# Kernel optimization log

Measured on AMD Instinct MI355X. Metric: run time of the kernel, lower is better.

The kernel has to match this reference:

```python
import jax, jax.numpy as jnp
import numpy as np

HIDDEN = 2048
NUM_HEADS = 16
NUM_KV_HEADS = 4
HEAD_DIM = HIDDEN // NUM_HEADS  # 128
WINDOW = 512
THETA = 10000.0
BATCH = 4
SEQ = 2048
NEG = -1e30


def _apply_rope(x, pos, theta):
    # x: [T, H, D] with interleaved even/odd rotation, matching the torch strided slicing
    half = x.shape[-1] // 2
    inv_freq = 1.0 / (theta ** (jnp.arange(half, dtype=jnp.float32) / half))
    ang = pos.astype(jnp.float32)[:, None] * inv_freq[None, :]          # [T, half]
    cos = jnp.cos(ang)[:, None, :]                                       # [T, 1, half]
    sin = jnp.sin(ang)[:, None, :]
    xe = x[..., 0::2].astype(jnp.float32)
    xo = x[..., 1::2].astype(jnp.float32)
    re = xe * cos - xo * sin
    ro = xe * sin + xo * cos
    out = jnp.stack([re, ro], axis=-1).reshape(x.shape)                  # re-interleave
    return out.astype(x.dtype)


def setup_inputs() -> dict:
    key = jax.random.key(0)
    ks = jax.random.split(key, 5)
    sc = 1.0 / np.sqrt(HIDDEN)
    hidden_states = jax.random.normal(ks[0], (BATCH * SEQ, HIDDEN), dtype=jnp.float32)
    q_w = jax.random.normal(ks[1], (HIDDEN, NUM_HEADS * HEAD_DIM), dtype=jnp.float32) * sc
    k_w = jax.random.normal(ks[2], (HIDDEN, NUM_KV_HEADS * HEAD_DIM), dtype=jnp.float32) * sc
    v_w = jax.random.normal(ks[3], (HIDDEN, NUM_KV_HEADS * HEAD_DIM), dtype=jnp.float32) * sc
    o_w = jax.random.normal(ks[4], (HIDDEN, HIDDEN), dtype=jnp.float32) * sc
    position_ids = jnp.tile(jnp.arange(SEQ, dtype=jnp.int32), BATCH)     # restart per sequence
    cu_seqlens = jnp.arange(BATCH + 1, dtype=jnp.int32) * SEQ
    return {
        "hidden_states": hidden_states, "q_w": q_w, "k_w": k_w, "v_w": v_w, "o_w": o_w,
        "position_ids": position_ids, "cu_seqlens": cu_seqlens, "max_seq_len": SEQ,
    }


def reference(hidden_states, q_w, k_w, v_w, o_w, position_ids, cu_seqlens, max_seq_len):
    T = hidden_states.shape[0]
    B = cu_seqlens.shape[0] - 1
    S = T // B  # equal-length packing
    groups = NUM_HEADS // NUM_KV_HEADS

    q = (hidden_states @ q_w).reshape(T, NUM_HEADS, HEAD_DIM)
    k = (hidden_states @ k_w).reshape(T, NUM_KV_HEADS, HEAD_DIM)
    v = (hidden_states @ v_w).reshape(T, NUM_KV_HEADS, HEAD_DIM)

    q = _apply_rope(q, position_ids, THETA)
    k = _apply_rope(k, position_ids, THETA)

    q = q.reshape(B, S, NUM_HEADS, HEAD_DIM)
    k = k.reshape(B, S, NUM_KV_HEADS, HEAD_DIM)
    v = v.reshape(B, S, NUM_KV_HEADS, HEAD_DIM)
    # GQA: expand kv heads to query heads
    k = jnp.repeat(k, groups, axis=2)   # [B, S, H, D]
    v = jnp.repeat(v, groups, axis=2)

    scale = 1.0 / np.sqrt(HEAD_DIM)
    scores = jnp.einsum('bqhd,bkhd->bhqk', q, k) * scale  # [B, H, S, S]

    pos = position_ids.reshape(B, S)
    pq = pos[:, None, :, None]
    pk = pos[:, None, None, :]
    # causal + sliding window (flash window_size=(WINDOW, 0) semantics): q-k in [0, WINDOW]
    allowed = (pk <= pq) & ((pq - pk) <= WINDOW)
    scores = jnp.where(allowed, scores, NEG)

    probs = jax.nn.softmax(scores, axis=-1)
    attn = jnp.einsum('bhqk,bkhd->bqhd', probs, v)        # [B, S, H, D]
    attn = attn.reshape(T, HIDDEN)
    return attn @ o_w
```

## Files before the change

### kernel.cpp

```cpp
#include <hip/hip_runtime.h>
#include <hip/hip_bf16.h>
#include <cstdint>
#include <cstddef>

typedef __bf16 bf16;
typedef __bf16 bf16x2 __attribute__((ext_vector_type(2)));
typedef __bf16 bf16x8 __attribute__((ext_vector_type(8)));
typedef float  f32x4  __attribute__((ext_vector_type(4)));

#define HIDDEN 2048
#define NHEADS 16
#define NKV    4
#define HD     128
#define WINDOW 512

__device__ __forceinline__ void gld16(const void* g, void* s) {
  __builtin_amdgcn_global_load_lds((const __attribute__((address_space(1))) void*)g,
                                   (__attribute__((address_space(3))) void*)s, 16, 0, 0);
}

__device__ __forceinline__ f32x4 mfma16(bf16x8 a, bf16x8 b, f32x4 c) {
  return __builtin_amdgcn_mfma_f32_16x16x32_bf16(a, b, c, 0, 0, 0);
}

__device__ __forceinline__ void barrier_raw() {
  asm volatile("" ::: "memory");
  __builtin_amdgcn_s_barrier();
  asm volatile("" ::: "memory");
}

__global__ __launch_bounds__(256) void cast_f32_bf16(const float* __restrict__ in,
                                                     bf16* __restrict__ out, int n4) {
  int i = blockIdx.x * 256 + threadIdx.x;
  if (i >= n4) return;
  f32x4 v = *(const f32x4*)(in + (size_t)i * 4);
  bf16x2 a, b;
  a[0] = (bf16)v[0]; a[1] = (bf16)v[1];
  b[0] = (bf16)v[2]; b[1] = (bf16)v[3];
  *(bf16x2*)(out + (size_t)i * 4)     = a;
  *(bf16x2*)(out + (size_t)i * 4 + 2) = b;
}

__global__ __launch_bounds__(256) void transpose_cast(const float* __restrict__ in,
                                                      bf16* __restrict__ out, int R, int C) {
  __shared__ float tile[32][33];
  int c0 = blockIdx.x * 32, r0 = blockIdx.y * 32;
  int tx = threadIdx.x, ty = threadIdx.y;
  #pragma unroll
  for (int i = 0; i < 4; ++i)
    tile[ty + i * 8][tx] = in[(size_t)(r0 + ty + i * 8) * C + c0 + tx];
  __syncthreads();
  #pragma unroll
  for (int i = 0; i < 4; ++i)
    out[(size_t)(c0 + ty + i * 8) * R + r0 + tx] = (bf16)tile[tx][ty + i * 8];
}

__device__ __forceinline__ void stage128x32(const bf16* __restrict__ A,
                                            const bf16* __restrict__ Bt,
                                            bf16* sA, bf16* sB,
                                            int m0, int n0, int K, int kt, int tid) {
  int wbase = tid & ~63;
  #pragma unroll
  for (int r = 0; r < 2; ++r) {
    int e = (r * 256 + tid) * 8;
    int row = e >> 5, col = e & 31;
    gld16(A  + (size_t)(m0 + row) * K + (size_t)kt * 32 + col,
          sA + (size_t)(r * 256 + wbase) * 8);
    gld16(Bt + (size_t)(n0 + row) * K + (size_t)kt * 32 + col,
          sB + (size_t)(r * 256 + wbase) * 8);
  }
}

__global__ __launch_bounds__(256) void gemm_bt(const bf16* __restrict__ A,
                                               const bf16* __restrict__ Bt,
                                               void* __restrict__ Cv,
                                               bf16* __restrict__ Vtout,
                                               int M, int N, int K, int outMode) {
  __shared__ bf16 sA[2][128 * 32];
  __shared__ bf16 sB[2][128 * 32];
  int nb = N >> 7;
  int perx = (int)gridDim.x >> 3;
  int bid0 = (int)blockIdx.x;
  int swzb = (bid0 & 7) * perx + (bid0 >> 3);
  int bm = swzb / nb, bn = swzb % nb;
  int m0 = bm << 7, n0 = bn << 7;
  int tid = threadIdx.x;
  int lane = tid & 63, w = tid >> 6;
  int li = lane & 15, g = lane >> 4, g8 = g * 8;
  int wm = w >> 1, wn = w & 1;
  f32x4 acc[4][4] = {};
  int NT = K >> 5;

  stage128x32(A, Bt, sA[0], sB[0], m0, n0, K, 0, tid);
  for (int kt = 0; kt < NT; ++kt) {
    int cur = kt & 1;
    asm volatile("s_waitcnt vmcnt(0)" ::: "memory");
    barrier_raw();
    if (kt + 1 < NT)
      stage128x32(A, Bt, sA[cur ^ 1], sB[cur ^ 1], m0, n0, K, kt + 1, tid);
    bf16x8 af[4], bv[4];
    #pragma unroll
    for (int mt = 0; mt < 4; ++mt)
      af[mt] = *(const bf16x8*)&sA[cur][(wm * 64 + mt * 16 + li) * 32 + g8];
    #pragma unroll
    for (int nt = 0; nt < 4; ++nt)
      bv[nt] = *(const bf16x8*)&sB[cur][(wn * 64 + nt * 16 + li) * 32 + g8];
    #pragma unroll
    for (int mt = 0; mt < 4; ++mt)
      #pragma unroll
      for (int nt = 0; nt < 4; ++nt)
        acc[mt][nt] = mfma16(af[mt], bv[nt], acc[mt][nt]);
  }
  #pragma unroll
  for (int mt = 0; mt < 4; ++mt)
    #pragma unroll
    for (int nt = 0; nt < 4; ++nt)
      #pragma unroll
      for (int j = 0; j < 4; ++j) {
        int row = m0 + wm * 64 + mt * 16 + g * 4 + j;
        int col = n0 + wn * 64 + nt * 16 + li;
        float v = acc[mt][nt][j];
        if (outMode == 0)      ((bf16*)Cv)[(size_t)row * N + col] = (bf16)v;
        else if (outMode == 1) ((bf16*)Cv)[(size_t)col * M + row] = (bf16)v;
        else if (outMode == 2) ((float*)Cv)[(size_t)row * N + col] = v;
        else {
          if (col < 512) ((bf16*)Cv)[(size_t)row * 512 + col] = (bf16)v;
          else           Vtout[(size_t)(col - 512) * M + row] = (bf16)v;
        }
      }
}

template<int RSP>
__device__ __forceinline__ void stage_quad(const bf16* __restrict__ G,
                                           bf16* __restrict__ sbuf,
                                           int grow0, int K, int k0, int half, int tid) {
  int w = tid >> 6, lane = tid & 63;
  int rl = lane >> 3;
  int col = ((lane & 7) ^ rl) * 8;
  #pragma unroll
  for (int r = 0; r < 2; ++r) {
    int lr0 = r * 64 + w * 8;
    int row0 = (lr0 & (RSP - 1)) + half * RSP + (lr0 / RSP) * 2 * RSP;
    gld16(G + (size_t)(grow0 + row0 + rl) * K + k0 + col,
          sbuf + row0 * 64);
  }
}

__global__ __launch_bounds__(512, 2) void gemm256(const bf16* __restrict__ A,
                                                  const bf16* __restrict__ Bt,
                                                  void* __restrict__ Cv,
                                                  int M, int N, int K, int outMode) {
  __shared__ bf16 sA[2][256 * 64];
  __shared__ bf16 sB[2][256 * 64];
  int nb = N >> 8;
  int cpx = (int)gridDim.x >> 3;
  int bid = (int)blockIdx.x;
  int swzb = (bid & 7) * cpx + (bid >> 3);
  int bm = swzb / nb, bn = swzb % nb;
  int m0 = bm << 8, n0 = bn << 8;
  int tid = threadIdx.x, lane = tid & 63, w = tid >> 6;
  int li = lane & 15, g = lane >> 4;
  int wm = w >> 2, wn = w & 3;
  int swz = (li & 7);

  f32x4 acc[8][4] = {};
  bf16x8 af[4][2];
  bf16x8 bv[2][2][2];

  int NT = K >> 6;

  stage_quad<64>(A,  sA[0], m0, K, 0, 0, tid);
  stage_quad<32>(Bt, sB[0], n0, K, 0, 0, tid);
  stage_quad<32>(Bt, sB[0], n0, K, 0, 1, tid);
  stage_quad<64>(A,  sA[0], m0, K, 0, 1, tid);

#define VMW(n) asm volatile("s_waitcnt vmcnt(" #n ")" ::: "memory")
#define SBAR() __builtin_amdgcn_sched_barrier(0)
#define LGKM(n) { asm volatile("s_waitcnt lgkmcnt(" #n ")" ::: "memory"); \
  __builtin_amdgcn_sched_barrier(0); }
#define LOAD_A256(mh) { _Pragma("unroll") for (int mf = 0; mf < 4; ++mf) \
  _Pragma("unroll") for (int ks = 0; ks < 2; ++ks) { \
    int row = wm * 128 + (mh) * 64 + mf * 16 + li; \
    af[mf][ks] = *(const bf16x8*)&sA[cur][row * 64 + ((ks * 4 + g) ^ swz) * 8]; } }
#define LOAD_B256(nh) { _Pragma("unroll") for (int nf = 0; nf < 2; ++nf) \
  _Pragma("unroll") for (int ks = 0; ks < 2; ++ks) { \
    int row = wn * 64 + (nh) * 32 + nf * 16 + li; \
    bv[nh][nf][ks] = *(const bf16x8*)&sB[cur][row * 64 + ((ks * 4 + g) ^ swz) * 8]; } }
#define MFMA_PH(mh, nh) { \
  __builtin_amdgcn_s_setprio(1); \
  _Pragma("unroll") for (int mf = 0; mf < 4; ++mf) \
  _Pragma("unroll") for (int nf = 0; nf < 2; ++nf) \
  _Pragma("unroll") for (int ks = 0; ks < 2; ++ks) \
    acc[(mh) * 4 + mf][(nh) * 2 + nf] = \
      mfma16(af[mf][ks], bv[nh][nf][ks], acc[(mh) * 4 + mf][(nh) * 2 + nf]); \
  __builtin_amdgcn_s_setprio(0); }

  int cur = 0;
  for (int t = 0; t < NT; ++t) {
    int nxt = cur ^ 1;
    bool pre = (t + 1 < NT);
    int k1 = (t + 1) << 6;
    VMW(0);
    barrier_raw();
    if (pre) stage_quad<64>(A, sA[nxt], m0, K, k1, 0, tid);
    LOAD_A256(0); LOAD_B256(0);
    SBAR();
    LOAD_B256(1);
    if (pre) stage_quad<32>(Bt, sB[nxt], n0, K, k1, 0, tid);
    LGKM(4);
    MFMA_PH(0, 0);
    if (pre) stage_quad<32>(Bt, sB[nxt], n0, K, k1, 1, tid);
    LGKM(0);
    MFMA_PH(0, 1);
    LOAD_A256(1);
    if (pre) stage_quad<64>(A, sA[nxt], m0, K, k1, 1, tid);
    LGKM(0);
    MFMA_PH(1, 1);
    MFMA_PH(1, 0);
    cur = nxt;
  }
#undef VMW
#undef SBAR
#undef LGKM
#undef LOAD_A256
#undef LOAD_B256
#undef MFMA_PH

  #pragma unroll
  for (int mi = 0; mi < 8; ++mi)
    #pragma unroll
    for (int ni = 0; ni < 4; ++ni)
      #pragma unroll
      for (int j = 0; j < 4; ++j) {
        int row = m0 + wm * 128 + mi * 16 + g * 4 + j;
        int col = n0 + wn * 64 + ni * 16 + li;
        float v = acc[mi][ni][j];
        if (outMode == 2) ((float*)Cv)[(size_t)row * N + col] = v;
        else              ((bf16*)Cv)[(size_t)row * N + col] = (bf16)v;
      }
}

__global__ __launch_bounds__(256) void rope_kernel(bf16* __restrict__ X,
                                                   const int* __restrict__ pos,
                                                   int T, int heads) {
  int idx = blockIdx.x * 256 + threadIdx.x;
  int total = T * heads * 64;
  if (idx >= total) return;
  int i = idx & 63;
  int rest = idx >> 6;
  int hh = rest % heads;
  int t = rest / heads;
  float inv = expf((float)i * (-9.210340371976184f / 64.0f));
  float ang = (float)pos[t] * inv;
  float s, c;
  sincosf(ang, &s, &c);
  bf16* p = X + ((size_t)t * heads + hh) * HD + 2 * i;
  bf16x2 xv = *(const bf16x2*)p;
  float xe = (float)xv[0], xo = (float)xv[1];
  bf16x2 r;
  r[0] = (bf16)(xe * c - xo * s);
  r[1] = (bf16)(xe * s + xo * c);
  *(bf16x2*)p = r;
}

__global__ __launch_bounds__(512) void attn_kernel(const bf16* __restrict__ Q,
                                                   const bf16* __restrict__ Kb,
                                                   const bf16* __restrict__ Vt,
                                                   const int* __restrict__ pos,
                                                   const int* __restrict__ cu,
                                                   bf16* __restrict__ O, int T, int B) {
  __shared__ bf16 sK[2][32 * 128];
  __shared__ bf16 sVt2[2][64 * 64];
  __shared__ bf16 sP[8][16 * 40];
  int bid = blockIdx.x;
  int nqb = T >> 6;
  int kvh = bid / nqb;
  int u   = bid % nqb;
  int qb  = (u & 7) * (nqb >> 3) + (u >> 3);
  int q0 = qb * 64;
  int tid = threadIdx.x, lane = tid & 63, w = tid >> 6;
  int hh = w & 3, rh = w >> 2;
  int h = kvh * 4 + hh;
  int li = lane & 15, g = lane >> 4, g8 = g * 8;
  int rb0 = q0 + rh * 32;

  int seq_start = 0, seq_end = T;
  for (int b = 0; b < B; ++b) {
    int a = cu[b], e = cu[b + 1];
    if (q0 >= a && q0 < e) { seq_start = a; seq_end = e; }
  }

  bf16x8 qf[2][4];
  #pragma unroll
  for (int grp = 0; grp < 2; ++grp)
    #pragma unroll
    for (int kd = 0; kd < 4; ++kd)
      qf[grp][kd] = *(const bf16x8*)(Q + (size_t)(rb0 + grp * 16 + li) * HIDDEN
                                     + h * HD + kd * 32 + g8);

  int pq[2][4], pmin[2], pmax[2];
  #pragma unroll
  for (int grp = 0; grp < 2; ++grp) {
    #pragma unroll
    for (int j = 0; j < 4; ++j) pq[grp][j] = pos[rb0 + grp * 16 + g * 4 + j];
    pmin[grp] = pos[rb0 + grp * 16];
    pmax[grp] = pos[rb0 + grp * 16 + 15];
  }

  float lsum[2][4] = {};
  f32x4 acc[2][8] = {};
  int kstart = q0 - WINDOW;
  if (kstart < seq_start) kstart = seq_start;
  int kend = q0 + 64;
  if (kend > seq_end) kend = seq_end;
  const float scale = 0.08838834764831845f;
  int nt = (kend - kstart) >> 5;

  int krow = tid >> 4, kc = (tid & 15) ^ (krow & 7);
  int vr = tid >> 3, vc = (tid & 7) ^ (vr & 7);
  int vd = 2 * vr + (vc >> 2), vkey = (vc & 3) * 8;
  int wbase = (tid & ~63) * 8;

#define STAGE(kb_, buf_) { \
  gld16(Kb + (size_t)((kb_) + krow) * (NKV * HD) + kvh * HD + kc * 8, \
        &sK[buf_][wbase]); \
  gld16(Vt + (size_t)(kvh * HD + vd) * T + (kb_) + vkey, \
        &sVt2[buf_][wbase]); }
#define VMW(n) asm volatile("s_waitcnt vmcnt(" #n ")" ::: "memory")

  STAGE(kstart, 0);
  for (int t = 0; t < nt; ++t) {
    int kb = kstart + t * 32;
    int cur = t & 1;
    VMW(0);
    barrier_raw();
    if (t + 1 < nt) STAGE(kb + 32, cur ^ 1);

    int pkf = pos[kb], pkl = pos[kb + 31];
    int pk0 = pos[kb + li], pk1 = pos[kb + 16 + li];
    #pragma unroll
    for (int grp = 0; grp < 2; ++grp) {
      if (pkf > pmax[grp] || pkl < pmin[grp] - WINDOW) continue;
      f32x4 s0v = {0.f, 0.f, 0.f, 0.f}, s1v = {0.f, 0.f, 0.f, 0.f};
      #pragma unroll
      for (int kd = 0; kd < 4; ++kd) {
        int c0 = (kd * 4 + g) ^ (li & 7);
        bf16x8 b0 = *(const bf16x8*)&sK[cur][li * 128 + c0 * 8];
        bf16x8 b1 = *(const bf16x8*)&sK[cur][(16 + li) * 128 + c0 * 8];
        s0v = mfma16(qf[grp][kd], b0, s0v);
        s1v = mfma16(qf[grp][kd], b1, s1v);
      }
      bool interior = (pkl <= pmin[grp]) && (pmax[grp] - pkf <= WINDOW);
      if (interior) {
        #pragma unroll
        for (int j = 0; j < 4; ++j) {
          float p0 = __expf(s0v[j] * scale);
          float p1 = __expf(s1v[j] * scale);
          lsum[grp][j] += p0 + p1;
          sP[w][(g * 4 + j) * 40 + li]      = (bf16)p0;
          sP[w][(g * 4 + j) * 40 + 16 + li] = (bf16)p1;
        }
      } else {
        #pragma unroll
        for (int j = 0; j < 4; ++j) {
          int d0 = pq[grp][j] - pk0, d1 = pq[grp][j] - pk1;
          float p0 = (d0 >= 0 && d0 <= WINDOW) ? __expf(s0v[j] * scale) : 0.f;
          float p1 = (d1 >= 0 && d1 <= WINDOW) ? __expf(s1v[j] * scale) : 0.f;
          lsum[grp][j] += p0 + p1;
          sP[w][(g * 4 + j) * 40 + li]      = (bf16)p0;
          sP[w][(g * 4 + j) * 40 + 16 + li] = (bf16)p1;
        }
      }
      bf16x8 pa = *(const bf16x8*)&sP[w][li * 40 + g8];
      #pragma unroll
      for (int dt = 0; dt < 8; ++dt) {
        int d = dt * 16 + li;
        int vr2 = d >> 1;
        int vc2 = ((d & 1) * 4 + g) ^ (vr2 & 7);
        bf16x8 vf = *(const bf16x8*)&sVt2[cur][vr2 * 64 + vc2 * 8];
        acc[grp][dt] = mfma16(pa, vf, acc[grp][dt]);
      }
    }
  }
#undef STAGE
#undef VMW

  #pragma unroll
  for (int grp = 0; grp < 2; ++grp)
    #pragma unroll
    for (int j = 0; j < 4; ++j) {
      float rs = lsum[grp][j];
      rs += __shfl_xor(rs, 1);
      rs += __shfl_xor(rs, 2);
      rs += __shfl_xor(rs, 4);
      rs += __shfl_xor(rs, 8);
      float invl = 1.0f / rs;
      size_t base = (size_t)(rb0 + grp * 16 + g * 4 + j) * HIDDEN + h * HD;
      #pragma unroll
      for (int dt = 0; dt < 8; ++dt)
        O[base + dt * 16 + li] = (bf16)(acc[grp][dt][j] * invl);
    }
}

extern "C" void kernel_launch(void* const* d_in, const int* in_sizes, int n_in,
                              void* d_out, int out_size, void* d_ws, size_t ws_size,
                              hipStream_t stream) {
  const float* X  = (const float*)d_in[0];
  const float* qw = (const float*)d_in[1];
  const float* kw = (const float*)d_in[2];
  const float* vw = (const float*)d_in[3];
  const float* ow = (const float*)d_in[4];
  const int* pos = (const int*)d_in[5];
  const int* cu  = (const int*)d_in[6];
  int T = in_sizes[0] / HIDDEN;
  int B = in_sizes[6] - 1;
  float* out = (float*)d_out;

  bf16* ws = (bf16*)d_ws;
  size_t off = 0;
  bf16* Xb    = ws + off; off += (size_t)T * HIDDEN;
  bf16* Qb    = ws + off; off += (size_t)T * HIDDEN;
  bf16* Kb    = ws + off; off += (size_t)T * (NKV * HD);
  bf16* Vt    = ws + off; off += (size_t)T * (NKV * HD);
  bf16* qwT   = ws + off; off += (size_t)HIDDEN * HIDDEN;
  bf16* kvwT  = ws + off; off += (size_t)1024 * HIDDEN;
  bf16* owT   = ws + off; off += (size_t)HIDDEN * HIDDEN;

  cast_f32_bf16<<<(T * HIDDEN / 4 + 255) / 256, 256, 0, stream>>>(X, Xb, T * HIDDEN / 4);

  dim3 tb(32, 8);
  transpose_cast<<<dim3(HIDDEN / 32, HIDDEN / 32), tb, 0, stream>>>(qw, qwT, HIDDEN, HIDDEN);
  transpose_cast<<<dim3(512 / 32, HIDDEN / 32), tb, 0, stream>>>(kw, kvwT, HIDDEN, 512);
  transpose_cast<<<dim3(512 / 32, HIDDEN / 32), tb, 0, stream>>>(vw, kvwT + (size_t)512 * HIDDEN, HIDDEN, 512);
  transpose_cast<<<dim3(HIDDEN / 32, HIDDEN / 32), tb, 0, stream>>>(ow, owT, HIDDEN, HIDDEN);

  gemm256<<<(T / 256) * (HIDDEN / 256), 512, 0, stream>>>(Xb, qwT, Qb, T, HIDDEN, HIDDEN, 0);
  gemm_bt<<<(T / 128) * (1024 / 128), 256, 0, stream>>>(Xb, kvwT, Kb, Vt, T, 1024, HIDDEN, 3);

  rope_kernel<<<(T * NHEADS * 64 + 255) / 256, 256, 0, stream>>>(Qb, pos, T, NHEADS);
  rope_kernel<<<(T * NKV * 64 + 255) / 256, 256, 0, stream>>>(Kb, pos, T, NKV);

  attn_kernel<<<(T / 64) * NKV, 512, 0, stream>>>(Qb, Kb, Vt, pos, cu, Qb, T, B);

  gemm256<<<(T / 256) * (HIDDEN / 256), 512, 0, stream>>>(Qb, owT, out, T, HIDDEN, HIDDEN, 2);
}
```

Measured before the change: 333.1 us.

## Stage 64-key K/V tiles per barrier in attention and fuse Q/K RoPE launches

The attention kernel now stages 64 keys per iteration instead of 32, doubling the K and V shared-memory buffers and splitting compute into two 32-key halves. The V tile layout changes from a paired-row packing to one row per head dimension with an XOR swizzle. The aim is to halve the number of barriers and wait points per KV sweep so each sync covers more work. The two RoPE launches are also merged into one kernel over both Q and K. The trade-off is roughly twice the LDS per block, which may lower occupancy, and the kv range must now be a multiple of 64.

```diff
diff --git a/kernel.cpp b/kernel.cpp
--- a/kernel.cpp
+++ b/kernel.cpp
@@ -240,14 +240,18 @@
       }
 }
 
-__global__ __launch_bounds__(256) void rope_kernel(bf16* __restrict__ X,
-                                                   const int* __restrict__ pos,
-                                                   int T, int heads) {
+__global__ __launch_bounds__(256) void rope_both(bf16* __restrict__ Qb,
+                                                 bf16* __restrict__ Kb,
+                                                 const int* __restrict__ pos, int T) {
   int idx = blockIdx.x * 256 + threadIdx.x;
-  int total = T * heads * 64;
+  int total_q = T * NHEADS * 64;
+  int total   = total_q + T * NKV * 64;
   if (idx >= total) return;
-  int i = idx & 63;
-  int rest = idx >> 6;
+  bf16* X; int heads, local;
+  if (idx < total_q) { X = Qb; heads = NHEADS; local = idx; }
+  else               { X = Kb; heads = NKV;    local = idx - total_q; }
+  int i = local & 63;
+  int rest = local >> 6;
   int hh = rest % heads;
   int t = rest / heads;
   float inv = expf((float)i * (-9.210340371976184f / 64.0f));
@@ -269,8 +273,8 @@
                                                    const int* __restrict__ pos,
                                                    const int* __restrict__ cu,
                                                    bf16* __restrict__ O, int T, int B) {
-  __shared__ bf16 sK[2][32 * 128];
-  __shared__ bf16 sVt2[2][64 * 64];
+  __shared__ bf16 sK[2][64 * 128];
+  __shared__ bf16 sV[2][128 * 64];
   __shared__ bf16 sP[8][16 * 40];
   int bid = blockIdx.x;
   int nqb = T >> 6;
@@ -314,71 +318,73 @@
   int kend = q0 + 64;
   if (kend > seq_end) kend = seq_end;
   const float scale = 0.08838834764831845f;
-  int nt = (kend - kstart) >> 5;
-
-  int krow = tid >> 4, kc = (tid & 15) ^ (krow & 7);
-  int vr = tid >> 3, vc = (tid & 7) ^ (vr & 7);
-  int vd = 2 * vr + (vc >> 2), vkey = (vc & 3) * 8;
-  int wbase = (tid & ~63) * 8;
+  int nt = (kend - kstart) >> 6;
 
 #define STAGE(kb_, buf_) { \
-  gld16(Kb + (size_t)((kb_) + krow) * (NKV * HD) + kvh * HD + kc * 8, \
-        &sK[buf_][wbase]); \
-  gld16(Vt + (size_t)(kvh * HD + vd) * T + (kb_) + vkey, \
-        &sVt2[buf_][wbase]); }
+  _Pragma("unroll") for (int r = 0; r < 2; ++r) { \
+    int n = r * 512 + tid; \
+    int krow = n >> 4, kc = (n & 15) ^ (krow & 7); \
+    gld16(Kb + (size_t)((kb_) + krow) * (NKV * HD) + kvh * HD + kc * 8, \
+          &sK[buf_][(size_t)(r * 512 + (tid & ~63)) * 8]); \
+    int vd = n >> 3, vc = (n & 7) ^ (vd & 7); \
+    gld16(Vt + (size_t)(kvh * HD + vd) * T + (kb_) + vc * 8, \
+          &sV[buf_][(size_t)(r * 512 + (tid & ~63)) * 8]); } }
 #define VMW(n) asm volatile("s_waitcnt vmcnt(" #n ")" ::: "memory")
 
   STAGE(kstart, 0);
   for (int t = 0; t < nt; ++t) {
-    int kb = kstart + t * 32;
+    int kb0 = kstart + t * 64;
     int cur = t & 1;
     VMW(0);
     barrier_raw();
-    if (t + 1 < nt) STAGE(kb + 32, cur ^ 1);
-
-    int pkf = pos[kb], pkl = pos[kb + 31];
-    int pk0 = pos[kb + li], pk1 = pos[kb + 16 + li];
-    #pragma unroll
-    for (int grp = 0; grp < 2; ++grp) {
-      if (pkf > pmax[grp] || pkl < pmin[grp] - WINDOW) continue;
-      f32x4 s0v = {0.f, 0.f, 0.f, 0.f}, s1v = {0.f, 0.f, 0.f, 0.f};
+    if (t + 1 < nt) STAGE(kb0 + 64, cur ^ 1);
+
+    #pragma unroll
+    for (int hhalf = 0; hhalf < 2; ++hhalf) {
+      int kb = kb0 + hhalf * 32;
+      int pkf = pos[kb], pkl = pos[kb + 31];
+      int pk0 = pos[kb + li], pk1 = pos[kb + 16 + li];
       #pragma unroll
-      for (int kd = 0; kd < 4; ++kd) {
-        int c0 = (kd * 4 + g) ^ (li & 7);
-        bf16x8 b0 = *(const bf16x8*)&sK[cur][li * 128 + c0 * 8];
-        bf16x8 b1 = *(const bf16x8*)&sK[cur][(16 + li) * 128 + c0 * 8];
-        s0v = mfma16(qf[grp][kd], b0, s0v);
-        s1v = mfma16(qf[grp][kd], b1, s1v);
-      }
-      bool interior = (pkl <= pmin[grp]) && (pmax[grp] - pkf <= WINDOW);
-      if (interior) {
+      for (int grp = 0; grp < 2; ++grp) {
+        if (pkf > pmax[grp] || pkl < pmin[grp] - WINDOW) continue;
+        f32x4 s0v = {0.f, 0.f, 0.f, 0.f}, s1v = {0.f, 0.f, 0.f, 0.f};
         #pragma unroll
-        for (int j = 0; j < 4; ++j) {
-          float p0 = __expf(s0v[j] * scale);
-          float p1 = __expf(s1v[j] * scale);
-          lsum[grp][j] += p0 + p1;
-          sP[w][(g * 4 + j) * 40 + li]      = (bf16)p0;
-          sP[w][(g * 4 + j) * 40 + 16 + li] = (bf16)p1;
+        for (int kd = 0; kd < 4; ++kd) {
+          int c0 = (kd * 4 + g) ^ (li & 7);
+          bf16x8 b0 = *(const bf16x8*)&sK[cur][(hhalf * 32 + li) * 128 + c0 * 8];
+          bf16x8 b1 = *(const bf16x8*)&sK[cur][(hhalf * 32 + 16 + li) * 128 + c0 * 8];
+          s0v = mfma16(qf[grp][kd], b0, s0v);
+          s1v = mfma16(qf[grp][kd], b1, s1v);
         }
-      } else {
+        bool interior = (pkl <= pmin[grp]) && (pmax[grp] - pkf <= WINDOW);
+        if (interior) {
+          #pragma unroll
+          for (int j = 0; j < 4; ++j) {
+            float p0 = __expf(s0v[j] * scale);
+            float p1 = __expf(s1v[j] * scale);
+            lsum[grp][j] += p0 + p1;
+            sP[w][(g * 4 + j) * 40 + li]      = (bf16)p0;
+            sP[w][(g * 4 + j) * 40 + 16 + li] = (bf16)p1;
+          }
+        } else {
+          #pragma unroll
+          for (int j = 0; j < 4; ++j) {
+            int d0 = pq[grp][j] - pk0, d1 = pq[grp][j] - pk1;
+            float p0 = (d0 >= 0 && d0 <= WINDOW) ? __expf(s0v[j] * scale) : 0.f;
+            float p1 = (d1 >= 0 && d1 <= WINDOW) ? __expf(s1v[j] * scale) : 0.f;
+            lsum[grp][j] += p0 + p1;
+            sP[w][(g * 4 + j) * 40 + li]      = (bf16)p0;
+            sP[w][(g * 4 + j) * 40 + 16 + li] = (bf16)p1;
+          }
+        }
+        bf16x8 pa = *(const bf16x8*)&sP[w][li * 40 + g8];
         #pragma unroll
-        for (int j = 0; j < 4; ++j) {
-          int d0 = pq[grp][j] - pk0, d1 = pq[grp][j] - pk1;
-          float p0 = (d0 >= 0 && d0 <= WINDOW) ? __expf(s0v[j] * scale) : 0.f;
-          float p1 = (d1 >= 0 && d1 <= WINDOW) ? __expf(s1v[j] * scale) : 0.f;
-          lsum[grp][j] += p0 + p1;
-          sP[w][(g * 4 + j) * 40 + li]      = (bf16)p0;
-          sP[w][(g * 4 + j) * 40 + 16 + li] = (bf16)p1;
+        for (int dt = 0; dt < 8; ++dt) {
+          int d = dt * 16 + li;
+          int vc2 = (hhalf * 4 + g) ^ (d & 7);
+          bf16x8 vf = *(const bf16x8*)&sV[cur][d * 64 + vc2 * 8];
+          acc[grp][dt] = mfma16(pa, vf, acc[grp][dt]);
         }
-      }
-      bf16x8 pa = *(const bf16x8*)&sP[w][li * 40 + g8];
-      #pragma unroll
-      for (int dt = 0; dt < 8; ++dt) {
-        int d = dt * 16 + li;
-        int vr2 = d >> 1;
-        int vc2 = ((d & 1) * 4 + g) ^ (vr2 & 7);
-        bf16x8 vf = *(const bf16x8*)&sVt2[cur][vr2 * 64 + vc2 * 8];
-        acc[grp][dt] = mfma16(pa, vf, acc[grp][dt]);
       }
     }
   }
@@ -437,8 +443,7 @@
   gemm256<<<(T / 256) * (HIDDEN / 256), 512, 0, stream>>>(Xb, qwT, Qb, T, HIDDEN, HIDDEN, 0);
   gemm_bt<<<(T / 128) * (1024 / 128), 256, 0, stream>>>(Xb, kvwT, Kb, Vt, T, 1024, HIDDEN, 3);
 
-  rope_kernel<<<(T * NHEADS * 64 + 255) / 256, 256, 0, stream>>>(Qb, pos, T, NHEADS);
-  rope_kernel<<<(T * NKV * 64 + 255) / 256, 256, 0, stream>>>(Kb, pos, T, NKV);
+  rope_both<<<(T * (NHEADS + NKV) * 64 + 255) / 256, 256, 0, stream>>>(Qb, Kb, pos, T);
 
   attn_kernel<<<(T / 64) * NKV, 512, 0, stream>>>(Qb, Kb, Vt, pos, cu, Qb, T, B);
 
```

Measured after the change: 320.5 us. 3.8% less time.
